# Kernel tuning notes

Hardware: AMD Instinct MI355X
Metric: run time of the kernel (lower is better)

Reference implementation:

```python
import jax, jax.numpy as jnp
import numpy as np

B, S, H, NH, HD = 2, 2048, 4096, 32, 128
THETA = 10000.0


def rotate_half(x):
    x1, x2 = jnp.split(x, 2, axis=-1)
    return jnp.concatenate((-x2, x1), axis=-1)


def setup_inputs() -> dict:
    key = jax.random.key(0)
    ks = jax.random.split(key, 6)
    hidden_states = jax.random.normal(ks[0], (B, S, H), dtype=jnp.float32)
    # additive causal mask, [1,1,S,S]
    causal = jnp.triu(jnp.full((S, S), -1e9, dtype=jnp.float32), k=1)
    attention_mask = causal[None, None, :, :]
    scale = 0.02
    Wq = jax.random.normal(ks[1], (H, H), dtype=jnp.float32) * scale
    Wk = jax.random.normal(ks[2], (H, H), dtype=jnp.float32) * scale
    Wv = jax.random.normal(ks[3], (H, H), dtype=jnp.float32) * scale
    Wo = jax.random.normal(ks[4], (H, H), dtype=jnp.float32) * scale
    return {"hidden_states": hidden_states, "attention_mask": attention_mask,
            "Wq": Wq, "Wk": Wk, "Wv": Wv, "Wo": Wo}


def _rope_tables(seq_len, dtype):
    inv_freq = 1.0 / (THETA ** (jnp.arange(0, HD, 2, dtype=jnp.float32) / HD))
    t = jnp.arange(seq_len, dtype=jnp.float32)
    freqs = jnp.einsum('i,j->ij', t, inv_freq)          # [S, HD/2]
    emb = jnp.concatenate((freqs, freqs), axis=-1)       # [S, HD]
    return jnp.cos(emb).astype(dtype), jnp.sin(emb).astype(dtype)


def reference(hidden_states, attention_mask, Wq, Wk, Wv, Wo):
    b, s, _ = hidden_states.shape
    # nn.Linear: y = x @ W.T
    q = jnp.einsum('bsh,oh->bso', hidden_states, Wq).reshape(b, s, NH, HD).transpose(0, 2, 1, 3)
    k = jnp.einsum('bsh,oh->bso', hidden_states, Wk).reshape(b, s, NH, HD).transpose(0, 2, 1, 3)
    v = jnp.einsum('bsh,oh->bso', hidden_states, Wv).reshape(b, s, NH, HD).transpose(0, 2, 1, 3)
    cos, sin = _rope_tables(s, q.dtype)                  # [S, HD] broadcast over b,h
    q = q * cos + rotate_half(q) * sin
    k = k * cos + rotate_half(k) * sin
    scores = jnp.einsum('bhqd,bhkd->bhqk', q, k) / jnp.sqrt(jnp.asarray(HD, q.dtype))
    scores = scores + attention_mask
    attn = jax.nn.softmax(scores.astype(jnp.float32), axis=-1).astype(q.dtype)
    out = jnp.einsum('bhqk,bhkd->bhqd', attn, v)
    out = out.transpose(0, 2, 1, 3).reshape(b, s, H)
    return jnp.einsum('bsh,oh->bso', out, Wo)
```

## Files before the change

### kernel.cpp

```cpp
#include <hip/hip_runtime.h>
#include <stdint.h>

typedef __attribute__((ext_vector_type(4))) float f32x4;
typedef __attribute__((ext_vector_type(8))) short bf16x8;
typedef __attribute__((ext_vector_type(4))) unsigned int u32x4;

__device__ __forceinline__ short f2bf(float x) {
  unsigned int u = __builtin_bit_cast(unsigned int, x);
  unsigned int r = (u + 0x7fffu + ((u >> 16) & 1u)) >> 16;
  return (short)r;
}
__device__ __forceinline__ float bf2f(short s) {
  unsigned int u = ((unsigned int)(unsigned short)s) << 16;
  return __builtin_bit_cast(float, u);
}
__device__ __forceinline__ unsigned pkbf(float lo, float hi) {
  unsigned r;
  asm("v_cvt_pk_bf16_f32 %0, %1, %2" : "=v"(r) : "v"(lo), "v"(hi));
  return r;
}

__device__ __forceinline__ void gload_lds16(const void* g, void* l) {
  __builtin_amdgcn_global_load_lds(
      (const __attribute__((address_space(1))) void*)g,
      (__attribute__((address_space(3))) void*)l, 16, 0, 0);
}

__global__ __launch_bounds__(256) void cvt5(const float* __restrict__ a,
                                            const float* __restrict__ b,
                                            const float* __restrict__ c,
                                            const float* __restrict__ d,
                                            const float* __restrict__ e,
                                            short* __restrict__ oa,
                                            short* __restrict__ ob,
                                            short* __restrict__ oc,
                                            short* __restrict__ od,
                                            short* __restrict__ oe, int n) {
  int y = blockIdx.y;
  const float* in = (y == 0) ? a : (y == 1) ? b : (y == 2) ? c : (y == 3) ? d : e;
  short* out = (y == 0) ? oa : (y == 1) ? ob : (y == 2) ? oc : (y == 3) ? od : oe;
  int idx = blockIdx.x * blockDim.x + threadIdx.x;
  int stride = gridDim.x * blockDim.x;
  for (int i = idx * 4; i < n; i += stride * 4) {
    float4 v = *(const float4*)(in + i);
    short4 o;
    o.x = f2bf(v.x); o.y = f2bf(v.y); o.z = f2bf(v.z); o.w = f2bf(v.w);
    *(short4*)(out + i) = o;
  }
}

__global__ __launch_bounds__(256) void cvt_bf16(const float* __restrict__ in,
                                                short* __restrict__ out, int n) {
  int idx = blockIdx.x * blockDim.x + threadIdx.x;
  int stride = gridDim.x * blockDim.x;
  for (int i = idx * 4; i < n; i += stride * 4) {
    float4 v = *(const float4*)(in + i);
    short4 o;
    o.x = f2bf(v.x); o.y = f2bf(v.y); o.z = f2bf(v.z); o.w = f2bf(v.w);
    *(short4*)(out + i) = o;
  }
}

__global__ __launch_bounds__(256) void rope_table_k(float2* __restrict__ tab) {
  int idx = blockIdx.x * 256 + threadIdx.x;
  int s = idx >> 6, j = idx & 63;
  float invf = powf(10000.0f, -((float)j) / 64.0f);
  float a = (float)s * invf;
  tab[idx] = make_float2(cosf(a), sinf(a));
}

__global__ __launch_bounds__(256) void rope_apply_k(short* __restrict__ Qb,
                                                    short* __restrict__ Kb,
                                                    const float2* __restrict__ tab) {
  bool isK = (blockIdx.y != 0);
  short* base = isK ? Kb : Qb;
  float post = isK ? 1.0f : (0.08838834764831845f * 1.4426950408889634f);
  int token = blockIdx.x;
  int s = token & 2047;
  short* rowp = base + (size_t)token * 4096;
  const float2* trow = tab + s * 64;
  for (int u = threadIdx.x; u < 512; u += 256) {
    int h = u >> 4;
    int d0 = (u & 15) * 4;
    short* p1 = rowp + h * 128 + d0;
    short* p2 = p1 + 64;
    short4 a = *(short4*)p1, b = *(short4*)p2;
    short4 ra, rb;
#pragma unroll
    for (int j = 0; j < 4; ++j) {
      short aj = (&a.x)[j], bj = (&b.x)[j];
      float qa = bf2f(aj), qb = bf2f(bj);
      float2 cs = trow[d0 + j];
      (&ra.x)[j] = f2bf((qa * cs.x - qb * cs.y) * post);
      (&rb.x)[j] = f2bf((qb * cs.x + qa * cs.y) * post);
    }
    *(short4*)p1 = ra;
    *(short4*)p2 = rb;
  }
}

template <int MODE>
__global__ __launch_bounds__(512) void gemm8p(const short* __restrict__ A,
                                              const short* __restrict__ Bw,
                                              void* __restrict__ out) {
  __shared__ __attribute__((aligned(16))) short smem[2 * 32768];
  int wg = blockIdx.x;
  int xcd = wg & 7, ii = wg >> 3;
  int by = xcd * 2 + (ii >> 4);
  int bx = ii & 15;
  int tid = threadIdx.x;
  int w = tid >> 6, lane = tid & 63;
  int l16 = lane & 15, l4 = lane >> 4;
  int wm = w >> 2, wn = w & 3;

  f32x4 acc[8][4] = {};

  const short* Ab = A + (size_t)(by * 256) * 4096;
  const short* Bb = Bw + (size_t)(bx * 256) * 4096;

  auto STAGE_MAT = [&](int kt, int isB) {
    const short* src = isB ? Bb : Ab;
    int ob = (kt & 1) * 32768 + isB * 16384;
#pragma unroll
    for (int j = 0; j < 4; ++j) {
      int c = j * 512 + tid;
      int row = c >> 3;
      int sc = (c & 7) ^ (row & 7);
      gload_lds16(src + (size_t)row * 4096 + kt * 64 + sc * 8, &smem[ob + c * 8]);
    }
  };

  bf16x8 bfr[4];
  auto PHASE = [&](int ob, int kk, int mh, bool loadB) {
    const short* lA = &smem[ob];
    const short* lB = &smem[ob + 16384];
    if (loadB) {
#pragma unroll
      for (int nf = 0; nf < 4; ++nf) {
        int row = wn * 64 + nf * 16 + l16;
        int phys = (kk * 4 + l4) ^ (row & 7);
        bfr[nf] = *(const bf16x8*)&lB[row * 64 + phys * 8];
      }
    }
    bf16x8 af[4];
#pragma unroll
    for (int mf = 0; mf < 4; ++mf) {
      int row = wm * 128 + mh * 64 + mf * 16 + l16;
      int phys = (kk * 4 + l4) ^ (row & 7);
      af[mf] = *(const bf16x8*)&lA[row * 64 + phys * 8];
    }
    __builtin_amdgcn_s_setprio(1);
#pragma unroll
    for (int mf = 0; mf < 4; ++mf)
#pragma unroll
      for (int nf = 0; nf < 4; ++nf)
        acc[mh * 4 + mf][nf] =
            __builtin_amdgcn_mfma_f32_16x16x32_bf16(af[mf], bfr[nf], acc[mh * 4 + mf][nf], 0, 0, 0);
    __builtin_amdgcn_s_setprio(0);
    __builtin_amdgcn_s_barrier();
    asm volatile("" ::: "memory");
  };

  STAGE_MAT(0, 0);
  STAGE_MAT(0, 1);
  asm volatile("s_waitcnt vmcnt(0)" ::: "memory");
  __builtin_amdgcn_s_barrier();
  asm volatile("" ::: "memory");

  const int b0 = 0, b1 = 32768;
  for (int i = 0; i < 32; ++i) {
    int kt1 = 2 * i + 1;
    STAGE_MAT(kt1, 0);
    asm volatile("s_waitcnt vmcnt(4)" ::: "memory");
    __builtin_amdgcn_s_barrier();
    asm volatile("" ::: "memory");
    PHASE(b0, 0, 0, true);
    STAGE_MAT(kt1, 1);
    PHASE(b0, 0, 1, false);
    PHASE(b0, 1, 0, true);
    PHASE(b0, 1, 1, false);
    if (i + 1 < 32) {
      STAGE_MAT(2 * i + 2, 0);
      asm volatile("s_waitcnt vmcnt(4)" ::: "memory");
    } else {
      asm volatile("s_waitcnt vmcnt(0)" ::: "memory");
    }
    __builtin_amdgcn_s_barrier();
    asm volatile("" ::: "memory");
    PHASE(b1, 0, 0, true);
    if (i + 1 < 32) STAGE_MAT(2 * i + 2, 1);
    PHASE(b1, 0, 1, false);
    PHASE(b1, 1, 0, true);
    PHASE(b1, 1, 1, false);
  }

  int orow0 = by * 256 + wm * 128;
  int ocol0 = bx * 256 + wn * 64;
#pragma unroll
  for (int mf = 0; mf < 8; ++mf)
#pragma unroll
    for (int nf = 0; nf < 4; ++nf)
#pragma unroll
      for (int k = 0; k < 4; ++k) {
        int r = orow0 + mf * 16 + l4 * 4 + k;
        int c = ocol0 + nf * 16 + l16;
        float v = acc[mf][nf][k];
        if constexpr (MODE == 0) {
          ((short*)out)[(size_t)r * 4096 + c] = f2bf(v);
        } else if constexpr (MODE == 1) {
          ((float*)out)[(size_t)r * 4096 + c] = v;
        } else {
          int bb = r >> 11, ss = r & 2047;
          int h = c >> 7, d = c & 127;
          ((short*)out)[(((size_t)((bb * 32 + h) * 128 + d)) << 11) + ss] = f2bf(v);
        }
      }
}

__global__ __launch_bounds__(256) void attn_k(const short* __restrict__ Qb,
                                              const short* __restrict__ Kb,
                                              const short* __restrict__ Vt,
                                              short* __restrict__ AO) {
  __shared__ __attribute__((aligned(16))) short smem[24576];
  int p = blockIdx.x;
  int bh = p & 63;
  int qt = 15 - (p >> 6);
  int b = bh >> 5, h = bh & 31;
  int tid = threadIdx.x, w = tid >> 6, lane = tid & 63;
  int l16 = lane & 15, l4 = lane >> 4;

  const int nt = 2 * qt + 2;
  const int qbase = qt * 128 + w * 32;

  bf16x8 qf[2][4];
  {
    const short* Qg = Qb + (size_t)(b * 2048 + qbase + l16) * 4096 + h * 128 + l4 * 8;
#pragma unroll
    for (int mg = 0; mg < 2; ++mg)
#pragma unroll
      for (int kk = 0; kk < 4; ++kk)
        qf[mg][kk] = *(const bf16x8*)(Qg + (size_t)mg * 16 * 4096 + kk * 32);
  }

  f32x4 oacc[2][8] = {};
  float mrun[2] = {-1e30f, -1e30f}, lsum[2] = {0.f, 0.f};

  const short* Kbase = Kb + (size_t)(b * 2048) * 4096 + h * 128;
  const short* Vbase = Vt + (size_t)bh * 128 * 2048;

  const int srowK = l4, skbK = l16;
  const int srowV = lane >> 3, skbV = lane & 7;

  auto STAGE_K = [&](int t, int sel) {
    short* lK = &smem[sel * 8192];
#pragma unroll
    for (int ii = 0; ii < 4; ++ii) {
      int s = w * 4 + ii;
      int rowK = s * 4 + srowK;
      int srcK = skbK ^ (rowK & 15);
      gload_lds16(Kbase + (size_t)(t * 64 + rowK) * 4096 + srcK * 8, &lK[s * 512]);
    }
  };
  auto STAGE_V = [&](int t) {
    short* lV = &smem[16384];
#pragma unroll
    for (int ii = 0; ii < 4; ++ii) {
      int s = w * 4 + ii;
      int rowV = s * 8 + srowV;
      int srcV = skbV ^ (rowV & 7);
      gload_lds16(Vbase + (size_t)rowV * 2048 + t * 64 + srcV * 8, &lV[s * 512]);
    }
  };

  STAGE_V(0);
  STAGE_K(0, 0);
  STAGE_K(1, 1);
  asm volatile("s_waitcnt vmcnt(4)" ::: "memory");
  __builtin_amdgcn_s_barrier();
  asm volatile("" ::: "memory");

  const int src0 = l16 | ((2 * (l4 & 1)) << 4);
  const int src1 = src0 | 16;
  const bool hiA = (l4 >> 1) != 0;

  for (int t = 0; t < nt; ++t) {
    const short* lK = &smem[(t & 1) * 8192];
    const short* lV = &smem[16384];
    bool skip = (t * 64 > qbase + 31);

    f32x4 sacc[2][4] = {};
    if (!skip) {
#pragma unroll
      for (int kk = 0; kk < 4; ++kk) {
#pragma unroll
        for (int n4 = 0; n4 < 4; ++n4) {
          int row = n4 * 16 + l16;
          int phys = (kk * 4 + l4) ^ (row & 15);
          bf16x8 kf = *(const bf16x8*)&lK[row * 128 + phys * 8];
          sacc[0][n4] = __builtin_amdgcn_mfma_f32_16x16x32_bf16(kf, qf[0][kk], sacc[0][n4], 0, 0, 0);
          sacc[1][n4] = __builtin_amdgcn_mfma_f32_16x16x32_bf16(kf, qf[1][kk], sacc[1][n4], 0, 0, 0);
        }
      }

      if (t * 64 + 63 > qbase) {
#pragma unroll
        for (int mg = 0; mg < 2; ++mg) {
          int q = qbase + mg * 16 + l16;
#pragma unroll
          for (int n4 = 0; n4 < 4; ++n4)
#pragma unroll
            for (int i = 0; i < 4; ++i) {
              int kv = t * 64 + n4 * 16 + l4 * 4 + i;
              if (kv > q) sacc[mg][n4][i] = -1e30f;
            }
        }
      }

#pragma unroll
      for (int mg = 0; mg < 2; ++mg) {
        float v0 = fmaxf(fmaxf(sacc[mg][0][0], sacc[mg][0][1]), fmaxf(sacc[mg][0][2], sacc[mg][0][3]));
        float v1 = fmaxf(fmaxf(sacc[mg][1][0], sacc[mg][1][1]), fmaxf(sacc[mg][1][2], sacc[mg][1][3]));
        float v2 = fmaxf(fmaxf(sacc[mg][2][0], sacc[mg][2][1]), fmaxf(sacc[mg][2][2], sacc[mg][2][3]));
        float v3 = fmaxf(fmaxf(sacc[mg][3][0], sacc[mg][3][1]), fmaxf(sacc[mg][3][2], sacc[mg][3][3]));
        float vm = fmaxf(fmaxf(v0, v1), fmaxf(v2, v3));
        vm = fmaxf(vm, __shfl_xor(vm, 16));
        vm = fmaxf(vm, __shfl_xor(vm, 32));
        float mn = mrun[mg];
        if (!__all(vm - mn <= 8.0f)) {
          float mnew = fmaxf(mn, vm);
          float fsc = __builtin_amdgcn_exp2f(mn - mnew);
          mrun[mg] = mnew;
          lsum[mg] *= fsc;
#pragma unroll
          for (int dg = 0; dg < 8; ++dg) oacc[mg][dg] *= fsc;
          mn = mnew;
        }
        float psum = 0.f;
#pragma unroll
        for (int n4 = 0; n4 < 4; ++n4)
#pragma unroll
          for (int i = 0; i < 4; ++i) {
            float e = __builtin_amdgcn_exp2f(sacc[mg][n4][i] - mn);
            sacc[mg][n4][i] = e;
            psum += e;
          }
        psum += __shfl_xor(psum, 16);
        psum += __shfl_xor(psum, 32);
        lsum[mg] += psum;
      }
    }

    if (t == nt - 1)
      asm volatile("s_waitcnt vmcnt(0)" ::: "memory");
    else
      asm volatile("s_waitcnt vmcnt(4)" ::: "memory");
    __builtin_amdgcn_s_barrier();
    asm volatile("" ::: "memory");

    if (!skip) {
      bf16x8 pb[2][2];
#pragma unroll
      for (int mg = 0; mg < 2; ++mg)
#pragma unroll
        for (int c = 0; c < 2; ++c) {
          unsigned pk0h0 = pkbf(sacc[mg][2 * c][0], sacc[mg][2 * c][1]);
          unsigned pk0h1 = pkbf(sacc[mg][2 * c][2], sacc[mg][2 * c][3]);
          unsigned pk1h0 = pkbf(sacc[mg][2 * c + 1][0], sacc[mg][2 * c + 1][1]);
          unsigned pk1h1 = pkbf(sacc[mg][2 * c + 1][2], sacc[mg][2 * c + 1][3]);
          unsigned s00 = __shfl((int)pk0h0, src0), s10 = __shfl((int)pk1h0, src0);
          unsigned s01 = __shfl((int)pk0h1, src0), s11 = __shfl((int)pk1h1, src0);
          unsigned t00 = __shfl((int)pk0h0, src1), t10 = __shfl((int)pk1h0, src1);
          unsigned t01 = __shfl((int)pk0h1, src1), t11 = __shfl((int)pk1h1, src1);
          u32x4 uw;
          uw[0] = hiA ? s10 : s00;
          uw[1] = hiA ? s11 : s01;
          uw[2] = hiA ? t10 : t00;
          uw[3] = hiA ? t11 : t01;
          pb[mg][c] = __builtin_bit_cast(bf16x8, uw);
        }

#pragma unroll
      for (int c = 0; c < 2; ++c)
#pragma unroll
        for (int dg = 0; dg < 8; ++dg) {
          int d = dg * 16 + l16;
          int phys = (c * 4 + l4) ^ (d & 7);
          bf16x8 vf = *(const bf16x8*)&lV[d * 64 + phys * 8];
          oacc[0][dg] = __builtin_amdgcn_mfma_f32_16x16x32_bf16(vf, pb[0][c], oacc[0][dg], 0, 0, 0);
          oacc[1][dg] = __builtin_amdgcn_mfma_f32_16x16x32_bf16(vf, pb[1][c], oacc[1][dg], 0, 0, 0);
        }
    }

    __builtin_amdgcn_s_barrier();
    asm volatile("" ::: "memory");
    if (t + 1 < nt) STAGE_V(t + 1);
    if (t + 2 < nt) STAGE_K(t + 2, t & 1);
    if (t + 2 < nt)
      asm volatile("s_waitcnt vmcnt(8)" ::: "memory");
    else if (t + 1 < nt)
      asm volatile("s_waitcnt vmcnt(4)" ::: "memory");
    __builtin_amdgcn_s_barrier();
    asm volatile("" ::: "memory");
  }

  short* reg = &smem[w * 4096];
  float rls0 = 1.0f / lsum[0], rls1 = 1.0f / lsum[1];
#pragma unroll
  for (int mg = 0; mg < 2; ++mg) {
    float rls = mg ? rls1 : rls0;
    int qloc = mg * 16 + l16;
#pragma unroll
    for (int dg = 0; dg < 8; ++dg) {
      unsigned u0 = pkbf(oacc[mg][dg][0] * rls, oacc[mg][dg][1] * rls);
      unsigned u1 = pkbf(oacc[mg][dg][2] * rls, oacc[mg][dg][3] * rls);
      int c16 = dg * 2 + (l4 >> 1);
      int phys = c16 ^ (qloc & 7);
      int sidx = qloc * 128 + phys * 8 + (l4 & 1) * 4;
      *(uint2*)&reg[sidx] = make_uint2(u0, u1);
    }
  }
#pragma unroll
  for (int pass = 0; pass < 8; ++pass) {
    int qloc = pass * 4 + l4;
    int phys = l16 ^ (qloc & 7);
    bf16x8 v = *(const bf16x8*)&reg[qloc * 128 + phys * 8];
    int qg = qt * 128 + w * 32 + qloc;
    *(bf16x8*)(AO + (size_t)(b * 2048 + qg) * 4096 + h * 128 + l16 * 8) = v;
  }
}

extern "C" void kernel_launch(void* const* d_in, const int* in_sizes, int n_in,
                              void* d_out, int out_size, void* d_ws, size_t ws_size,
                              hipStream_t stream) {
  const float* X = (const float*)d_in[0];
  const float* Wq = (const float*)d_in[2];
  const float* Wk = (const float*)d_in[3];
  const float* Wv = (const float*)d_in[4];
  const float* Wo = (const float*)d_in[5];

  char* ws = (char*)d_ws;
  const size_t SEG = 32ull << 20;
  short* Xb  = (short*)(ws + 0 * SEG);
  short* Wqb = (short*)(ws + 1 * SEG);
  short* Wkb = (short*)(ws + 2 * SEG);
  short* Wvb = (short*)(ws + 3 * SEG);
  short* Qb  = (short*)(ws + 4 * SEG);
  short* Kb  = (short*)(ws + 5 * SEG);
  float2* tab = (float2*)(ws + 6 * SEG);

  bool bigws = ws_size >= 6 * SEG + (4ull << 20) + SEG;
  short* WobBig = (short*)(ws + 6 * SEG + (4ull << 20));

  const int NE = 4096 * 4096;
  if (bigws) {
    cvt5<<<dim3(2048, 5), 256, 0, stream>>>(X, Wq, Wk, Wv, Wo, Xb, Wqb, Wkb, Wvb, WobBig, NE);
  } else {
    cvt5<<<dim3(2048, 4), 256, 0, stream>>>(X, Wq, Wk, Wv, nullptr, Xb, Wqb, Wkb, Wvb, nullptr, NE);
  }
  rope_table_k<<<512, 256, 0, stream>>>(tab);

  gemm8p<0><<<256, 512, 0, stream>>>(Xb, Wqb, Qb);
  gemm8p<0><<<256, 512, 0, stream>>>(Xb, Wkb, Kb);
  short* Vtb = Wqb;
  gemm8p<2><<<256, 512, 0, stream>>>(Xb, Wvb, Vtb);

  rope_apply_k<<<dim3(4096, 2), 256, 0, stream>>>(Qb, Kb, tab);

  short* AO = Xb;
  attn_k<<<1024, 256, 0, stream>>>(Qb, Kb, Vtb, AO);

  short* Wob;
  if (bigws) {
    Wob = WobBig;
  } else {
    Wob = Wkb;
    cvt_bf16<<<2048, 256, 0, stream>>>(Wo, Wob, NE);
  }
  gemm8p<1><<<256, 512, 0, stream>>>(AO, Wob, (float*)d_out);
}
```

Measured before the change: 735.0 us.

## Split attention query tile across eight waves of sixteen rows each

The attention kernel now launches 512 threads per block, so each of eight waves owns 16 query rows instead of four waves owning 32. This halves per-wave accumulator state, which should lower register pressure and permit more resident waves. The K/V staging is spread across all 512 threads, and the loop is restructured so one wait-plus-barrier sits at the top of each iteration instead of the mid-loop and end-of-loop sync pairs. In exchange, K/V LDS tiles are reused by fewer query rows per MFMA, so more LDS reads are issued per unit of compute, and the barriers now span more waves.

```diff
diff --git a/kernel.cpp b/kernel.cpp
--- a/kernel.cpp
+++ b/kernel.cpp
@@ -217,10 +217,10 @@
       }
 }
 
-__global__ __launch_bounds__(256) void attn_k(const short* __restrict__ Qb,
-                                              const short* __restrict__ Kb,
-                                              const short* __restrict__ Vt,
-                                              short* __restrict__ AO) {
+__global__ __launch_bounds__(512, 4) void attn_k(const short* __restrict__ Qb,
+                                                 const short* __restrict__ Kb,
+                                                 const short* __restrict__ Vt,
+                                                 short* __restrict__ AO) {
   __shared__ __attribute__((aligned(16))) short smem[24576];
   int p = blockIdx.x;
   int bh = p & 63;
@@ -230,66 +230,64 @@
   int l16 = lane & 15, l4 = lane >> 4;
 
   const int nt = 2 * qt + 2;
-  const int qbase = qt * 128 + w * 32;
-
-  bf16x8 qf[2][4];
+  const int qbase = qt * 128 + w * 16;
+
+  bf16x8 qf[4];
   {
     const short* Qg = Qb + (size_t)(b * 2048 + qbase + l16) * 4096 + h * 128 + l4 * 8;
 #pragma unroll
-    for (int mg = 0; mg < 2; ++mg)
-#pragma unroll
-      for (int kk = 0; kk < 4; ++kk)
-        qf[mg][kk] = *(const bf16x8*)(Qg + (size_t)mg * 16 * 4096 + kk * 32);
-  }
-
-  f32x4 oacc[2][8] = {};
-  float mrun[2] = {-1e30f, -1e30f}, lsum[2] = {0.f, 0.f};
+    for (int kk = 0; kk < 4; ++kk) qf[kk] = *(const bf16x8*)(Qg + kk * 32);
+  }
+
+  f32x4 oacc[8] = {};
+  float mrun = -1e30f, lsum = 0.f;
 
   const short* Kbase = Kb + (size_t)(b * 2048) * 4096 + h * 128;
   const short* Vbase = Vt + (size_t)bh * 128 * 2048;
 
-  const int srowK = l4, skbK = l16;
-  const int srowV = lane >> 3, skbV = lane & 7;
-
   auto STAGE_K = [&](int t, int sel) {
     short* lK = &smem[sel * 8192];
 #pragma unroll
-    for (int ii = 0; ii < 4; ++ii) {
-      int s = w * 4 + ii;
-      int rowK = s * 4 + srowK;
-      int srcK = skbK ^ (rowK & 15);
-      gload_lds16(Kbase + (size_t)(t * 64 + rowK) * 4096 + srcK * 8, &lK[s * 512]);
+    for (int j = 0; j < 2; ++j) {
+      int c = j * 512 + tid;
+      int row = c >> 4;
+      int src = (c & 15) ^ (row & 15);
+      gload_lds16(Kbase + (size_t)(t * 64 + row) * 4096 + src * 8, &lK[c * 8]);
     }
   };
   auto STAGE_V = [&](int t) {
     short* lV = &smem[16384];
 #pragma unroll
-    for (int ii = 0; ii < 4; ++ii) {
-      int s = w * 4 + ii;
-      int rowV = s * 8 + srowV;
-      int srcV = skbV ^ (rowV & 7);
-      gload_lds16(Vbase + (size_t)rowV * 2048 + t * 64 + srcV * 8, &lV[s * 512]);
+    for (int j = 0; j < 2; ++j) {
+      int c = j * 512 + tid;
+      int row = c >> 3;
+      int src = (c & 7) ^ (row & 7);
+      gload_lds16(Vbase + (size_t)row * 2048 + t * 64 + src * 8, &lV[c * 8]);
     }
   };
 
   STAGE_V(0);
   STAGE_K(0, 0);
   STAGE_K(1, 1);
-  asm volatile("s_waitcnt vmcnt(4)" ::: "memory");
-  __builtin_amdgcn_s_barrier();
-  asm volatile("" ::: "memory");
 
   const int src0 = l16 | ((2 * (l4 & 1)) << 4);
   const int src1 = src0 | 16;
   const bool hiA = (l4 >> 1) != 0;
 
   for (int t = 0; t < nt; ++t) {
-    const short* lK = &smem[(t & 1) * 8192];
-    const short* lV = &smem[16384];
-    bool skip = (t * 64 > qbase + 31);
-
-    f32x4 sacc[2][4] = {};
+    if (t == nt - 1)
+      asm volatile("s_waitcnt vmcnt(0)" ::: "memory");
+    else
+      asm volatile("s_waitcnt vmcnt(2)" ::: "memory");
+    __builtin_amdgcn_s_barrier();
+    asm volatile("" ::: "memory");
+
+    bool skip = (t * 64 > qbase + 15);
     if (!skip) {
+      const short* lK = &smem[(t & 1) * 8192];
+      const short* lV = &smem[16384];
+
+      f32x4 sacc[4] = {};
 #pragma unroll
       for (int kk = 0; kk < 4; ++kk) {
 #pragma unroll
@@ -297,135 +295,102 @@
           int row = n4 * 16 + l16;
           int phys = (kk * 4 + l4) ^ (row & 15);
           bf16x8 kf = *(const bf16x8*)&lK[row * 128 + phys * 8];
-          sacc[0][n4] = __builtin_amdgcn_mfma_f32_16x16x32_bf16(kf, qf[0][kk], sacc[0][n4], 0, 0, 0);
-          sacc[1][n4] = __builtin_amdgcn_mfma_f32_16x16x32_bf16(kf, qf[1][kk], sacc[1][n4], 0, 0, 0);
+          sacc[n4] = __builtin_amdgcn_mfma_f32_16x16x32_bf16(kf, qf[kk], sacc[n4], 0, 0, 0);
         }
       }
 
       if (t * 64 + 63 > qbase) {
-#pragma unroll
-        for (int mg = 0; mg < 2; ++mg) {
-          int q = qbase + mg * 16 + l16;
-#pragma unroll
-          for (int n4 = 0; n4 < 4; ++n4)
-#pragma unroll
-            for (int i = 0; i < 4; ++i) {
-              int kv = t * 64 + n4 * 16 + l4 * 4 + i;
-              if (kv > q) sacc[mg][n4][i] = -1e30f;
-            }
-        }
-      }
-
-#pragma unroll
-      for (int mg = 0; mg < 2; ++mg) {
-        float v0 = fmaxf(fmaxf(sacc[mg][0][0], sacc[mg][0][1]), fmaxf(sacc[mg][0][2], sacc[mg][0][3]));
-        float v1 = fmaxf(fmaxf(sacc[mg][1][0], sacc[mg][1][1]), fmaxf(sacc[mg][1][2], sacc[mg][1][3]));
-        float v2 = fmaxf(fmaxf(sacc[mg][2][0], sacc[mg][2][1]), fmaxf(sacc[mg][2][2], sacc[mg][2][3]));
-        float v3 = fmaxf(fmaxf(sacc[mg][3][0], sacc[mg][3][1]), fmaxf(sacc[mg][3][2], sacc[mg][3][3]));
+        int q = qbase + l16;
+#pragma unroll
+        for (int n4 = 0; n4 < 4; ++n4)
+#pragma unroll
+          for (int i = 0; i < 4; ++i) {
+            int kv = t * 64 + n4 * 16 + l4 * 4 + i;
+            if (kv > q) sacc[n4][i] = -1e30f;
+          }
+      }
+
+      {
+        float v0 = fmaxf(fmaxf(sacc[0][0], sacc[0][1]), fmaxf(sacc[0][2], sacc[0][3]));
+        float v1 = fmaxf(fmaxf(sacc[1][0], sacc[1][1]), fmaxf(sacc[1][2], sacc[1][3]));
+        float v2 = fmaxf(fmaxf(sacc[2][0], sacc[2][1]), fmaxf(sacc[2][2], sacc[2][3]));
+        float v3 = fmaxf(fmaxf(sacc[3][0], sacc[3][1]), fmaxf(sacc[3][2], sacc[3][3]));
         float vm = fmaxf(fmaxf(v0, v1), fmaxf(v2, v3));
         vm = fmaxf(vm, __shfl_xor(vm, 16));
         vm = fmaxf(vm, __shfl_xor(vm, 32));
-        float mn = mrun[mg];
-        if (!__all(vm - mn <= 8.0f)) {
-          float mnew = fmaxf(mn, vm);
-          float fsc = __builtin_amdgcn_exp2f(mn - mnew);
-          mrun[mg] = mnew;
-          lsum[mg] *= fsc;
-#pragma unroll
-          for (int dg = 0; dg < 8; ++dg) oacc[mg][dg] *= fsc;
-          mn = mnew;
+        if (!__all(vm - mrun <= 8.0f)) {
+          float mnew = fmaxf(mrun, vm);
+          float fsc = __builtin_amdgcn_exp2f(mrun - mnew);
+          mrun = mnew;
+          lsum *= fsc;
+#pragma unroll
+          for (int dg = 0; dg < 8; ++dg) oacc[dg] *= fsc;
         }
         float psum = 0.f;
 #pragma unroll
         for (int n4 = 0; n4 < 4; ++n4)
 #pragma unroll
           for (int i = 0; i < 4; ++i) {
-            float e = __builtin_amdgcn_exp2f(sacc[mg][n4][i] - mn);
-            sacc[mg][n4][i] = e;
+            float e = __builtin_amdgcn_exp2f(sacc[n4][i] - mrun);
+            sacc[n4][i] = e;
             psum += e;
           }
         psum += __shfl_xor(psum, 16);
         psum += __shfl_xor(psum, 32);
-        lsum[mg] += psum;
-      }
-    }
-
-    if (t == nt - 1)
-      asm volatile("s_waitcnt vmcnt(0)" ::: "memory");
-    else
-      asm volatile("s_waitcnt vmcnt(4)" ::: "memory");
-    __builtin_amdgcn_s_barrier();
-    asm volatile("" ::: "memory");
-
-    if (!skip) {
-      bf16x8 pb[2][2];
-#pragma unroll
-      for (int mg = 0; mg < 2; ++mg)
-#pragma unroll
-        for (int c = 0; c < 2; ++c) {
-          unsigned pk0h0 = pkbf(sacc[mg][2 * c][0], sacc[mg][2 * c][1]);
-          unsigned pk0h1 = pkbf(sacc[mg][2 * c][2], sacc[mg][2 * c][3]);
-          unsigned pk1h0 = pkbf(sacc[mg][2 * c + 1][0], sacc[mg][2 * c + 1][1]);
-          unsigned pk1h1 = pkbf(sacc[mg][2 * c + 1][2], sacc[mg][2 * c + 1][3]);
-          unsigned s00 = __shfl((int)pk0h0, src0), s10 = __shfl((int)pk1h0, src0);
-          unsigned s01 = __shfl((int)pk0h1, src0), s11 = __shfl((int)pk1h1, src0);
-          unsigned t00 = __shfl((int)pk0h0, src1), t10 = __shfl((int)pk1h0, src1);
-          unsigned t01 = __shfl((int)pk0h1, src1), t11 = __shfl((int)pk1h1, src1);
-          u32x4 uw;
-          uw[0] = hiA ? s10 : s00;
-          uw[1] = hiA ? s11 : s01;
-          uw[2] = hiA ? t10 : t00;
-          uw[3] = hiA ? t11 : t01;
-          pb[mg][c] = __builtin_bit_cast(bf16x8, uw);
-        }
-
-#pragma unroll
-      for (int c = 0; c < 2; ++c)
+        lsum += psum;
+      }
+
+#pragma unroll
+      for (int c = 0; c < 2; ++c) {
+        unsigned pk0h0 = pkbf(sacc[2 * c][0], sacc[2 * c][1]);
+        unsigned pk0h1 = pkbf(sacc[2 * c][2], sacc[2 * c][3]);
+        unsigned pk1h0 = pkbf(sacc[2 * c + 1][0], sacc[2 * c + 1][1]);
+        unsigned pk1h1 = pkbf(sacc[2 * c + 1][2], sacc[2 * c + 1][3]);
+        unsigned s00 = __shfl((int)pk0h0, src0), s10 = __shfl((int)pk1h0, src0);
+        unsigned s01 = __shfl((int)pk0h1, src0), s11 = __shfl((int)pk1h1, src0);
+        unsigned t00 = __shfl((int)pk0h0, src1), t10 = __shfl((int)pk1h0, src1);
+        unsigned t01 = __shfl((int)pk0h1, src1), t11 = __shfl((int)pk1h1, src1);
+        u32x4 uw;
+        uw[0] = hiA ? s10 : s00;
+        uw[1] = hiA ? s11 : s01;
+        uw[2] = hiA ? t10 : t00;
+        uw[3] = hiA ? t11 : t01;
+        bf16x8 pb = __builtin_bit_cast(bf16x8, uw);
 #pragma unroll
         for (int dg = 0; dg < 8; ++dg) {
           int d = dg * 16 + l16;
-          int phys = (c * 4 + l4) ^ (d & 7);
+          int phys = (c * 4 + l4) ^ (l16 & 7);
           bf16x8 vf = *(const bf16x8*)&lV[d * 64 + phys * 8];
-          oacc[0][dg] = __builtin_amdgcn_mfma_f32_16x16x32_bf16(vf, pb[0][c], oacc[0][dg], 0, 0, 0);
-          oacc[1][dg] = __builtin_amdgcn_mfma_f32_16x16x32_bf16(vf, pb[1][c], oacc[1][dg], 0, 0, 0);
+          oacc[dg] = __builtin_amdgcn_mfma_f32_16x16x32_bf16(vf, pb, oacc[dg], 0, 0, 0);
         }
+      }
     }
 
     __builtin_amdgcn_s_barrier();
     asm volatile("" ::: "memory");
     if (t + 1 < nt) STAGE_V(t + 1);
     if (t + 2 < nt) STAGE_K(t + 2, t & 1);
-    if (t + 2 < nt)
-      asm volatile("s_waitcnt vmcnt(8)" ::: "memory");
-    else if (t + 1 < nt)
-      asm volatile("s_waitcnt vmcnt(4)" ::: "memory");
-    __builtin_amdgcn_s_barrier();
-    asm volatile("" ::: "memory");
-  }
-
-  short* reg = &smem[w * 4096];
-  float rls0 = 1.0f / lsum[0], rls1 = 1.0f / lsum[1];
-#pragma unroll
-  for (int mg = 0; mg < 2; ++mg) {
-    float rls = mg ? rls1 : rls0;
-    int qloc = mg * 16 + l16;
-#pragma unroll
-    for (int dg = 0; dg < 8; ++dg) {
-      unsigned u0 = pkbf(oacc[mg][dg][0] * rls, oacc[mg][dg][1] * rls);
-      unsigned u1 = pkbf(oacc[mg][dg][2] * rls, oacc[mg][dg][3] * rls);
-      int c16 = dg * 2 + (l4 >> 1);
-      int phys = c16 ^ (qloc & 7);
-      int sidx = qloc * 128 + phys * 8 + (l4 & 1) * 4;
-      *(uint2*)&reg[sidx] = make_uint2(u0, u1);
-    }
-  }
-#pragma unroll
-  for (int pass = 0; pass < 8; ++pass) {
+  }
+
+  __syncthreads();
+  short* reg = &smem[w * 2048];
+  float rls = 1.0f / lsum;
+#pragma unroll
+  for (int dg = 0; dg < 8; ++dg) {
+    unsigned u0 = pkbf(oacc[dg][0] * rls, oacc[dg][1] * rls);
+    unsigned u1 = pkbf(oacc[dg][2] * rls, oacc[dg][3] * rls);
+    int cc = dg * 2 + (l4 >> 1);
+    int phys = cc ^ l16;
+    int sidx = l16 * 128 + phys * 8 + (l4 & 1) * 4;
+    *(uint2*)&reg[sidx] = make_uint2(u0, u1);
+  }
+#pragma unroll
+  for (int pass = 0; pass < 4; ++pass) {
     int qloc = pass * 4 + l4;
-    int phys = l16 ^ (qloc & 7);
+    int phys = l16 ^ qloc;
     bf16x8 v = *(const bf16x8*)&reg[qloc * 128 + phys * 8];
-    int qg = qt * 128 + w * 32 + qloc;
-    *(bf16x8*)(AO + (size_t)(b * 2048 + qg) * 4096 + h * 128 + l16 * 8) = v;
+    int tok = b * 2048 + qbase + qloc;
+    *(bf16x8*)(AO + (size_t)tok * 4096 + h * 128 + l16 * 8) = v;
   }
 }
 
@@ -467,7 +432,7 @@
   rope_apply_k<<<dim3(4096, 2), 256, 0, stream>>>(Qb, Kb, tab);
 
   short* AO = Xb;
-  attn_k<<<1024, 256, 0, stream>>>(Qb, Kb, Vtb, AO);
+  attn_k<<<1024, 512, 0, stream>>>(Qb, Kb, Vtb, AO);
 
   short* Wob;
   if (bigws) {
```

Result: faster. 676.3 us (-8.0%).
